# Optimization experiments

Hardware: AMD Instinct MI355X
Metric: run time of the kernel (lower is better)

Reference implementation:

```python
import jax, jax.numpy as jnp
import numpy as np
import math

B, S, D = 4, 2048, 1024
H, DK, DV = 16, 64, 64
EPS = 1e-5
SCALE = math.sqrt(1.0 / D)  # NOTE: original scales by 1/sqrt(d_model), not 1/sqrt(d_k)


def setup_inputs() -> dict:
    key = jax.random.key(0)
    ks = jax.random.split(key, 12)
    s = 0.02
    return {
        "Q": jax.random.normal(ks[0], (B, S, D), jnp.float32),
        "K": jax.random.normal(ks[1], (B, S, D), jnp.float32),
        "V": jax.random.normal(ks[2], (B, S, D), jnp.float32),
        # stacked per-head projection weights (torch Linear: y = x @ W.T + b)
        "Wq": jax.random.normal(ks[3], (H, D, DK), jnp.float32) * s,
        "bq": jnp.zeros((H, DK), jnp.float32),
        "Wk": jax.random.normal(ks[4], (H, D, DK), jnp.float32) * s,
        "bk": jnp.zeros((H, DK), jnp.float32),
        "Wv": jax.random.normal(ks[5], (H, D, DV), jnp.float32) * s,
        "bv": jnp.zeros((H, DV), jnp.float32),
        "Wo": jax.random.normal(ks[6], (H * DV, D), jnp.float32) * s,
        "bo": jnp.zeros((D,), jnp.float32),
        "gamma": jnp.ones((D,), jnp.float32),
        "beta": jnp.zeros((D,), jnp.float32),
    }


def reference(Q, K, V, Wq, bq, Wk, bk, Wv, bv, Wo, bo, gamma, beta):
    residual = Q
    # batched per-head projections: [B,S,D] x [H,D,dk] -> [B,H,S,dk]
    q = jnp.einsum("bsd,hdk->bhsk", Q, Wq) + bq[None, :, None, :]
    k = jnp.einsum("bsd,hdk->bhsk", K, Wk) + bk[None, :, None, :]
    v = jnp.einsum("bsd,hdv->bhsv", V, Wv) + bv[None, :, None, :]
    # scaled dot-product attention (scale uses d_model, per original code)
    attn = jax.nn.softmax(jnp.einsum("bhsk,bhtk->bhst", q, k) * SCALE, axis=-1)
    out = jnp.einsum("bhst,bhtv->bhsv", attn, v)  # [B,H,S,DV]
    # concat heads along feature dim: [B,S,H*DV]
    out = out.transpose(0, 2, 1, 3).reshape(B, S, H * DV)
    out = out @ Wo + bo  # output projection
    # dropout is identity in eval mode
    out = out + residual
    # BatchNorm1d over (B,S) per channel (training-mode batch stats)
    mean = jnp.mean(out, axis=(0, 1))
    var = jnp.mean(jnp.square(out - mean), axis=(0, 1))
    out = (out - mean) * jax.lax.rsqrt(var + EPS) * gamma + beta
    return out.transpose(0, 2, 1)  # (B, d_model, S)
```

## Files before the change

kernel.cpp:

```cpp
#include <hip/hip_runtime.h>

#define B_ 4
#define S_ 2048
#define D_ 1024
#define H_ 16
#define SCALE_ 0.03125f
#define EPS_ 1e-5f
#define NBS_ 8192

typedef unsigned short ushort_t;
typedef __attribute__((ext_vector_type(8))) short short8;
typedef __attribute__((ext_vector_type(4))) short short4v;
typedef __attribute__((ext_vector_type(4))) float floatx4;
typedef __attribute__((ext_vector_type(2))) unsigned int uint2v;

__device__ __forceinline__ ushort_t f2bf(float f) {
  union { float f; unsigned u; } v; v.f = f;
  unsigned r = v.u + 0x7fffu + ((v.u >> 16) & 1u);
  return (ushort_t)(r >> 16);
}

__device__ __forceinline__ float fast_exp2(float x) {
#if __has_builtin(__builtin_amdgcn_exp2f)
  return __builtin_amdgcn_exp2f(x);
#else
  return __expf(x * 0.6931471805599453f);
#endif
}

__device__ __forceinline__ unsigned cvt_pk_bf16(float a, float b) {
  unsigned r;
  asm("v_cvt_pk_bf16_f32 %0, %1, %2" : "=v"(r) : "v"(a), "v"(b));
  return r;
}

__device__ __forceinline__ short8 cvt8(float4 a, float4 b) {
  short8 r;
  r[0] = (short)f2bf(a.x); r[1] = (short)f2bf(a.y);
  r[2] = (short)f2bf(a.z); r[3] = (short)f2bf(a.w);
  r[4] = (short)f2bf(b.x); r[5] = (short)f2bf(b.y);
  r[6] = (short)f2bf(b.z); r[7] = (short)f2bf(b.w);
  return r;
}

__device__ __forceinline__ void gload16(const void* g, void* l) {
  __builtin_amdgcn_global_load_lds(
      (const __attribute__((address_space(1))) unsigned int*)g,
      (__attribute__((address_space(3))) unsigned int*)l, 16, 0, 0);
}

__global__ __launch_bounds__(256) void cvtx_k(const float* __restrict__ src,
                                              ushort_t* __restrict__ dst)
{
  size_t i = ((size_t)blockIdx.x * 256 + threadIdx.x) * 8;
  float4 a = *(const float4*)(src + i);
  float4 b = *(const float4*)(src + i + 4);
  *(short8*)(dst + i) = cvt8(a, b);
}

__global__ __launch_bounds__(256) void wtr_k(const float* __restrict__ src,
                                             ushort_t* __restrict__ dst, int mode)
{
  __shared__ float t[64][65];
  const int tr = blockIdx.x, tc = blockIdx.y;
  const float* sb; int sld;
  if (mode == 0) { sb = src + (size_t)tr * 65536 + (size_t)tc * 64 * 64; sld = 64; }
  else           { sb = src + (size_t)tc * 64 * 1024 + (size_t)tr * 64;  sld = 1024; }
  const int tid = threadIdx.x;
  const int rr = tid >> 2, cs = (tid & 3) * 16;
  const float* p = sb + (size_t)rr * sld + cs;
#pragma unroll
  for (int j = 0; j < 16; ++j) t[rr][cs + j] = p[j];
  __syncthreads();
  ushort_t* dp = dst + (size_t)(tr * 64 + rr) * 1024 + tc * 64 + cs;
#pragma unroll
  for (int j = 0; j < 16; ++j) dp[j] = f2bf(t[cs + j][rr]);
}

__global__ __launch_bounds__(256) void gemm_proj(
    const ushort_t* __restrict__ A, const ushort_t* __restrict__ Bw,
    const float* __restrict__ bias, ushort_t* __restrict__ outp, float scale)
{
  __shared__ ushort_t As[128 * 32];
  __shared__ ushort_t Bs[128 * 32];
  const int tid = threadIdx.x;
  const int wv = tid >> 6, lane = tid & 63, quad = lane >> 4, l16 = lane & 15;
  const int m0 = blockIdx.x * 128, n0 = blockIdx.y * 128;
  const int wm = wv & 1, wn = wv >> 1;
  const int lrow = lane >> 2, lkc = (lane & 3) * 8;

  floatx4 acc[4][4];
#pragma unroll
  for (int i = 0; i < 4; ++i)
#pragma unroll
    for (int j = 0; j < 4; ++j) acc[i][j] = (floatx4){0.f, 0.f, 0.f, 0.f};

  for (int k0 = 0; k0 < 1024; k0 += 32) {
    __syncthreads();
#pragma unroll
    for (int j = 0; j < 2; ++j) {
      const int rb = wv * 32 + j * 16;
      gload16(A + (size_t)(m0 + rb + lrow) * 1024 + k0 + lkc, (char*)As + rb * 64);
      gload16(Bw + (size_t)(n0 + rb + lrow) * 1024 + k0 + lkc, (char*)Bs + rb * 64);
    }
    __syncthreads();
    short8 af[4], bf[4];
#pragma unroll
    for (int i = 0; i < 4; ++i)
      af[i] = *(const short8*)&As[(wm * 64 + i * 16 + l16) * 32 + quad * 8];
#pragma unroll
    for (int i = 0; i < 4; ++i)
      bf[i] = *(const short8*)&Bs[(wn * 64 + i * 16 + l16) * 32 + quad * 8];
#pragma unroll
    for (int mi = 0; mi < 4; ++mi)
#pragma unroll
      for (int ni = 0; ni < 4; ++ni)
        acc[mi][ni] = __builtin_amdgcn_mfma_f32_16x16x32_bf16(
            af[mi], bf[ni], acc[mi][ni], 0, 0, 0);
  }

  const int b = m0 >> 11;
  const int sbase = (m0 & 2047) + wm * 64;
#pragma unroll
  for (int ni = 0; ni < 4; ++ni) {
    const int c = n0 + wn * 64 + ni * 16 + l16;
    const int h = c >> 6, nn = c & 63;
    const float bs = bias[c];
    ushort_t* op = outp + (size_t)(b * 16 + h) * 2048 * 64 + nn;
#pragma unroll
    for (int mi = 0; mi < 4; ++mi)
#pragma unroll
      for (int r = 0; r < 4; ++r) {
        int s = sbase + mi * 16 + quad * 4 + r;
        op[(size_t)s * 64] = f2bf((acc[mi][ni][r] + bs) * scale);
      }
  }
}

__global__ __launch_bounds__(256) void gemm_projT(
    const ushort_t* __restrict__ A, const ushort_t* __restrict__ Bw,
    const float* __restrict__ bias, ushort_t* __restrict__ outp)
{
  __shared__ ushort_t As[128 * 32];
  __shared__ ushort_t Bs[128 * 32];
  const int tid = threadIdx.x;
  const int wv = tid >> 6, lane = tid & 63, quad = lane >> 4, l16 = lane & 15;
  const int m0 = blockIdx.x * 128, n0 = blockIdx.y * 128;
  const int wm = wv & 1, wn = wv >> 1;
  const int lrow = lane >> 2, lkc = (lane & 3) * 8;

  floatx4 acc[4][4];
#pragma unroll
  for (int i = 0; i < 4; ++i)
#pragma unroll
    for (int j = 0; j < 4; ++j) acc[i][j] = (floatx4){0.f, 0.f, 0.f, 0.f};

  for (int k0 = 0; k0 < 1024; k0 += 32) {
    __syncthreads();
#pragma unroll
    for (int j = 0; j < 2; ++j) {
      const int rb = wv * 32 + j * 16;
      gload16(A + (size_t)(m0 + rb + lrow) * 1024 + k0 + lkc, (char*)As + rb * 64);
      gload16(Bw + (size_t)(n0 + rb + lrow) * 1024 + k0 + lkc, (char*)Bs + rb * 64);
    }
    __syncthreads();
    short8 af[4], bf[4];
#pragma unroll
    for (int i = 0; i < 4; ++i)
      af[i] = *(const short8*)&As[(wm * 64 + i * 16 + l16) * 32 + quad * 8];
#pragma unroll
    for (int i = 0; i < 4; ++i)
      bf[i] = *(const short8*)&Bs[(wn * 64 + i * 16 + l16) * 32 + quad * 8];
#pragma unroll
    for (int mi = 0; mi < 4; ++mi)
#pragma unroll
      for (int ni = 0; ni < 4; ++ni)
        acc[mi][ni] = __builtin_amdgcn_mfma_f32_16x16x32_bf16(
            af[mi], bf[ni], acc[mi][ni], 0, 0, 0);
  }

  const int b = m0 >> 11;
  const int sbase = (m0 & 2047) + wm * 64;
#pragma unroll
  for (int ni = 0; ni < 4; ++ni) {
    const int c = n0 + wn * 64 + ni * 16 + l16;
    const int h = c >> 6, nn = c & 63;
    const float bs = bias[c];
    ushort_t* op = outp + ((size_t)(b * 16 + h) * 64 + nn) * 2048;
#pragma unroll
    for (int mi = 0; mi < 4; ++mi) {
      int s0v = sbase + mi * 16 + quad * 4;
      short4v p;
#pragma unroll
      for (int r = 0; r < 4; ++r) p[r] = (short)f2bf(acc[mi][ni][r] + bs);
      *(short4v*)(op + s0v) = p;
    }
  }
}

__global__ __launch_bounds__(256) void gemm_oproj(
    const ushort_t* __restrict__ A, const ushort_t* __restrict__ Bw,
    const float* __restrict__ bo, const float* __restrict__ resid,
    float* __restrict__ y)
{
  __shared__ ushort_t As[128 * 32];
  __shared__ ushort_t Bs[128 * 32];
  const int tid = threadIdx.x;
  const int wv = tid >> 6, lane = tid & 63, quad = lane >> 4, l16 = lane & 15;
  const int m0 = blockIdx.x * 128, n0 = blockIdx.y * 128;
  const int wm = wv & 1, wn = wv >> 1;
  const int lrow = lane >> 2, lkc = (lane & 3) * 8;

  floatx4 acc[4][4];
#pragma unroll
  for (int i = 0; i < 4; ++i)
#pragma unroll
    for (int j = 0; j < 4; ++j) acc[i][j] = (floatx4){0.f, 0.f, 0.f, 0.f};

  for (int k0 = 0; k0 < 1024; k0 += 32) {
    __syncthreads();
#pragma unroll
    for (int j = 0; j < 2; ++j) {
      const int rb = wv * 32 + j * 16;
      gload16(A + (size_t)(m0 + rb + lrow) * 1024 + k0 + lkc, (char*)As + rb * 64);
      gload16(Bw + (size_t)(n0 + rb + lrow) * 1024 + k0 + lkc, (char*)Bs + rb * 64);
    }
    __syncthreads();
    short8 af[4], bf[4];
#pragma unroll
    for (int i = 0; i < 4; ++i)
      af[i] = *(const short8*)&As[(wm * 64 + i * 16 + l16) * 32 + quad * 8];
#pragma unroll
    for (int i = 0; i < 4; ++i)
      bf[i] = *(const short8*)&Bs[(wn * 64 + i * 16 + l16) * 32 + quad * 8];
#pragma unroll
    for (int mi = 0; mi < 4; ++mi)
#pragma unroll
      for (int ni = 0; ni < 4; ++ni)
        acc[mi][ni] = __builtin_amdgcn_mfma_f32_16x16x32_bf16(
            af[mi], bf[ni], acc[mi][ni], 0, 0, 0);
  }

  const int mb = m0 + wm * 64;
#pragma unroll
  for (int ni = 0; ni < 4; ++ni) {
    const int d = n0 + wn * 64 + ni * 16 + l16;
    const float bs = bo[d];
#pragma unroll
    for (int mi = 0; mi < 4; ++mi)
#pragma unroll
      for (int r = 0; r < 4; ++r) {
        int m = mb + mi * 16 + quad * 4 + r;
        y[(size_t)m * 1024 + d] = acc[mi][ni][r] + bs + resid[(size_t)m * 1024 + d];
      }
  }
}

__global__ __launch_bounds__(256, 3) void attn_k(
    const ushort_t* __restrict__ q, const ushort_t* __restrict__ k,
    const ushort_t* __restrict__ vt, ushort_t* __restrict__ ao)
{
  __shared__ ushort_t lds[24576];
  char* ldsb = (char*)lds;
  const int tid = threadIdx.x;
  const int wv = tid >> 6, lane = tid & 63, quad = lane >> 4, l16 = lane & 15;
  const int q0 = blockIdx.x * 128, h = blockIdx.y, b = blockIdx.z;
  const size_t bh = (size_t)(b * H_ + h) * S_;
  const ushort_t* vb = vt + (size_t)(b * H_ + h) * 64 * S_;

  short8 aq[2][2];
#pragma unroll
  for (int rb = 0; rb < 2; ++rb) {
    const ushort_t* qrow = q + (bh + q0 + wv * 32 + rb * 16 + l16) * 64;
    aq[rb][0] = *(const short8*)(qrow + quad * 8);
    aq[rb][1] = *(const short8*)(qrow + 32 + quad * 8);
  }

  short8 ones;
#pragma unroll
  for (int j = 0; j < 8; ++j) ones[j] = (short)0x3F80;

  floatx4 o[2][4];
  floatx4 accl[2];
#pragma unroll
  for (int rb = 0; rb < 2; ++rb) {
#pragma unroll
    for (int cb = 0; cb < 4; ++cb) o[rb][cb] = (floatx4){0.f, 0.f, 0.f, 0.f};
    accl[rb] = (floatx4){0.f, 0.f, 0.f, 0.f};
  }

  const int swz = ((l16 & 7) << 4) | (l16 & 8);
  const int q8 = quad * 8;
  const int pb = 32768 + wv * 4096 + l16 * 128;

  auto stage = [&](int nb, int t0) {
#pragma unroll
    for (int i = 0; i < 4; ++i) {
      const int idx = wv * 4 + i;
      const int cb = (idx >> 1) & 3, hf = idx & 1;
      if (idx < 8)
        gload16(k + (bh + t0 + cb * 16 + l16) * 64 + hf * 32 + quad * 8,
                (char*)lds + nb * 8192 + idx * 1024);
      else
        gload16(vb + (size_t)(cb * 16 + l16) * S_ + t0 + hf * 32 + quad * 8,
                (char*)lds + 16384 + nb * 8192 + (idx - 8) * 1024);
    }
  };

  stage(0, 0);
  asm volatile("s_waitcnt vmcnt(0)" ::: "memory");
  __syncthreads();

  for (int t0 = 0; t0 < S_; t0 += 64) {
    const int nb = (t0 >> 6) & 1;
    const ushort_t* KsC = lds + nb * 4096;
    const ushort_t* VsC = lds + 8192 + nb * 4096;
    if (t0 + 64 < S_) stage(nb ^ 1, t0 + 64);

    floatx4 sc[2][4];
#pragma unroll
    for (int rb = 0; rb < 2; ++rb)
#pragma unroll
      for (int cb = 0; cb < 4; ++cb) sc[rb][cb] = (floatx4){0.f, 0.f, 0.f, 0.f};
    __builtin_amdgcn_s_setprio(1);
#pragma unroll
    for (int hf = 0; hf < 2; ++hf) {
      short8 bk[4];
#pragma unroll
      for (int cb = 0; cb < 4; ++cb)
        bk[cb] = *(const short8*)&KsC[(cb * 2 + hf) * 512 + lane * 8];
#pragma unroll
      for (int rb = 0; rb < 2; ++rb)
#pragma unroll
        for (int cb = 0; cb < 4; ++cb)
          sc[rb][cb] = __builtin_amdgcn_mfma_f32_16x16x32_bf16(
              bk[cb], aq[rb][hf], sc[rb][cb], 0, 0, 0);
    }
    __builtin_amdgcn_s_setprio(0);

    short8 bvf[2][4];
#pragma unroll
    for (int hf = 0; hf < 2; ++hf)
#pragma unroll
      for (int cb = 0; cb < 4; ++cb)
        bvf[hf][cb] = *(const short8*)&VsC[(cb * 2 + hf) * 512 + lane * 8];

#pragma unroll
    for (int rb = 0; rb < 2; ++rb)
#pragma unroll
      for (int cb = 0; cb < 4; ++cb) {
        float p0 = fast_exp2(sc[rb][cb][0]);
        float p1 = fast_exp2(sc[rb][cb][1]);
        float p2 = fast_exp2(sc[rb][cb][2]);
        float p3 = fast_exp2(sc[rb][cb][3]);
        uint2v w;
        w[0] = cvt_pk_bf16(p0, p1);
        w[1] = cvt_pk_bf16(p2, p3);
        *(uint2v*)(ldsb + pb + rb * 2048 + ((cb * 32 + q8) ^ swz)) = w;
      }
    asm volatile("s_waitcnt lgkmcnt(0)" ::: "memory");
    __builtin_amdgcn_sched_barrier(0);

    __builtin_amdgcn_s_setprio(1);
#pragma unroll
    for (int rb = 0; rb < 2; ++rb)
#pragma unroll
      for (int hf = 0; hf < 2; ++hf) {
        const char* pr = ldsb + pb + rb * 2048;
        const int lo = (hf * 64 + quad * 16) ^ swz;
        short4v a0 = *(const short4v*)(pr + lo);
        short4v a1 = *(const short4v*)(pr + (lo ^ 8));
        short8 ap;
        ap[0] = a0[0]; ap[1] = a0[1]; ap[2] = a0[2]; ap[3] = a0[3];
        ap[4] = a1[0]; ap[5] = a1[1]; ap[6] = a1[2]; ap[7] = a1[3];
#pragma unroll
        for (int cb = 0; cb < 4; ++cb)
          o[rb][cb] = __builtin_amdgcn_mfma_f32_16x16x32_bf16(
              ap, bvf[hf][cb], o[rb][cb], 0, 0, 0);
        accl[rb] = __builtin_amdgcn_mfma_f32_16x16x32_bf16(
            ap, ones, accl[rb], 0, 0, 0);
      }
    __builtin_amdgcn_s_setprio(0);

    asm volatile("s_waitcnt vmcnt(0)" ::: "memory");
    __syncthreads();
  }

  float linv[2][4];
#pragma unroll
  for (int rb = 0; rb < 2; ++rb)
#pragma unroll
    for (int r = 0; r < 4; ++r)
      linv[rb][r] = 1.f / accl[rb][r];
#pragma unroll
  for (int rb = 0; rb < 2; ++rb)
#pragma unroll
    for (int cb = 0; cb < 4; ++cb)
#pragma unroll
      for (int r = 0; r < 4; ++r) {
        float val = o[rb][cb][r] * linv[rb][r];
        size_t idx = (size_t)(b * S_ + q0 + wv * 32 + rb * 16 + quad * 4 + r) * 1024
                     + h * 64 + cb * 16 + l16;
        ao[idx] = f2bf(val);
      }
}

__global__ __launch_bounds__(256) void stats_k(
    const float* __restrict__ y, float* __restrict__ s1, float* __restrict__ s2)
{
  const int tid = threadIdx.x;
  const int r0 = blockIdx.x * 32;
  float a[4] = {0.f, 0.f, 0.f, 0.f}, bb[4] = {0.f, 0.f, 0.f, 0.f};
  for (int r = 0; r < 32; ++r) {
    const float* row = y + (size_t)(r0 + r) * D_;
#pragma unroll
    for (int j = 0; j < 4; ++j) {
      float vv = row[tid + j * 256];
      a[j] += vv;
      bb[j] += vv * vv;
    }
  }
#pragma unroll
  for (int j = 0; j < 4; ++j) {
    atomicAdd(&s1[tid + j * 256], a[j]);
    atomicAdd(&s2[tid + j * 256], bb[j]);
  }
}

__global__ __launch_bounds__(256) void norm_k(
    const float* __restrict__ y, const float* __restrict__ s1,
    const float* __restrict__ s2, const float* __restrict__ gamma,
    const float* __restrict__ beta, float* __restrict__ out)
{
  __shared__ float tile[64][65];
  __shared__ float scl[64], sft[64];
  const int tid = threadIdx.x;
  const int s0 = blockIdx.x * 64, d0 = blockIdx.y * 64, b = blockIdx.z;

  if (tid < 64) {
    int d = d0 + tid;
    float mean = s1[d] * (1.f / (float)NBS_);
    float var = s2[d] * (1.f / (float)NBS_) - mean * mean;
    float rstd = rsqrtf(var + EPS_);
    float g = gamma[d];
    scl[tid] = rstd * g;
    sft[tid] = beta[d] - mean * rstd * g;
  }
  __syncthreads();

  const int si = tid >> 2, dc = (tid & 3) * 16;
  const float* row = y + (size_t)(b * S_ + s0 + si) * D_ + d0 + dc;
#pragma unroll
  for (int j = 0; j < 16; ++j)
    tile[si][dc + j] = row[j] * scl[dc + j] + sft[dc + j];
  __syncthreads();

  const int di = tid >> 2, sg = (tid & 3) * 16;
  float* dst = out + (size_t)(b * D_ + d0 + di) * S_ + s0 + sg;
#pragma unroll
  for (int jj = 0; jj < 4; ++jj) {
    float4 p;
    p.x = tile[sg + jj * 4 + 0][di];
    p.y = tile[sg + jj * 4 + 1][di];
    p.z = tile[sg + jj * 4 + 2][di];
    p.w = tile[sg + jj * 4 + 3][di];
    *(float4*)(dst + jj * 4) = p;
  }
}

extern "C" void kernel_launch(void* const* d_in, const int* in_sizes, int n_in,
                              void* d_out, int out_size, void* d_ws, size_t ws_size,
                              hipStream_t stream)
{
  (void)in_sizes; (void)n_in; (void)out_size; (void)ws_size;
  const float* Q     = (const float*)d_in[0];
  const float* Kin   = (const float*)d_in[1];
  const float* Vin   = (const float*)d_in[2];
  const float* Wq    = (const float*)d_in[3];
  const float* bq    = (const float*)d_in[4];
  const float* Wk    = (const float*)d_in[5];
  const float* bk    = (const float*)d_in[6];
  const float* Wv    = (const float*)d_in[7];
  const float* bv    = (const float*)d_in[8];
  const float* Wo    = (const float*)d_in[9];
  const float* bo    = (const float*)d_in[10];
  const float* gamma = (const float*)d_in[11];
  const float* beta  = (const float*)d_in[12];
  float* out = (float*)d_out;

  char* ws = (char*)d_ws;
  const size_t MB = 1u << 20;
  ushort_t* xb  = (ushort_t*)(ws);
  ushort_t* wtq = (ushort_t*)(ws + 16 * MB);
  ushort_t* wtk = (ushort_t*)(ws + 18 * MB);
  ushort_t* wtv = (ushort_t*)(ws + 20 * MB);
  ushort_t* wto = (ushort_t*)(ws + 22 * MB);
  ushort_t* qb  = (ushort_t*)(ws + 24 * MB);
  ushort_t* kb  = (ushort_t*)(ws + 40 * MB);
  ushort_t* vtb = (ushort_t*)(ws + 56 * MB);
  ushort_t* ao  = (ushort_t*)(ws);
  float*    y   = (float*)(ws + 24 * MB);
  float*    s1  = (float*)(ws + 56 * MB);
  float*    s2  = (float*)(ws + 56 * MB + 4096);

  wtr_k<<<dim3(16, 16), 256, 0, stream>>>(Wq, wtq, 0);
  wtr_k<<<dim3(16, 16), 256, 0, stream>>>(Wk, wtk, 0);
  wtr_k<<<dim3(16, 16), 256, 0, stream>>>(Wv, wtv, 0);
  wtr_k<<<dim3(16, 16), 256, 0, stream>>>(Wo, wto, 1);

  const float QSC = SCALE_ * 1.44269504088896f;
  cvtx_k<<<4096, 256, 0, stream>>>(Q, xb);
  gemm_proj<<<dim3(64, 8), 256, 0, stream>>>(xb, wtq, bq, qb, QSC);
  cvtx_k<<<4096, 256, 0, stream>>>(Kin, xb);
  gemm_proj<<<dim3(64, 8), 256, 0, stream>>>(xb, wtk, bk, kb, 1.0f);
  cvtx_k<<<4096, 256, 0, stream>>>(Vin, xb);
  gemm_projT<<<dim3(64, 8), 256, 0, stream>>>(xb, wtv, bv, vtb);

  attn_k<<<dim3(16, 16, 4), 256, 0, stream>>>(qb, kb, vtb, ao);
  gemm_oproj<<<dim3(64, 8), 256, 0, stream>>>(ao, wto, bo, Q, y);

  hipMemsetAsync(ws + 56 * MB, 0, 8192, stream);
  stats_k<<<256, 256, 0, stream>>>(y, s1, s2);
  norm_k<<<dim3(32, 16, 4), 256, 0, stream>>>(y, s1, s2, gamma, beta, out);
}
```

Before: 400.6 us.

## Double-buffer GEMM mainloop with swizzled LDS and fuse batchnorm stats into output projection

Replaces the three GEMM mainloops with a shared double-buffered loop using a K-tile of 64 and an XOR-swizzled LDS layout, so the next tile's global loads overlap the current tile's MFMAs and LDS bank conflicts drop. It also folds the per-channel sum and sum-of-squares into the output-projection epilogue via shuffles and atomics, which removes the separate stats kernel and its re-read of y. The cost is 64KB of LDS per GEMM block, which may reduce occupancy, and more atomic traffic from the epilogue.

```diff
diff --git a/kernel.cpp b/kernel.cpp
--- a/kernel.cpp
+++ b/kernel.cpp
@@ -77,17 +77,67 @@
   for (int j = 0; j < 16; ++j) dp[j] = f2bf(t[cs + j][rr]);
 }
 
+__device__ __forceinline__ void gemm_mainloop(
+    const ushort_t* __restrict__ A, const ushort_t* __restrict__ Bw,
+    ushort_t* As, ushort_t* Bs,
+    int m0, int n0, int wv, int lane, floatx4 acc[4][4])
+{
+  const int quad = lane >> 4, l16 = lane & 15;
+  const int wm = wv & 1, wn = wv >> 1;
+  const int r8 = lane >> 3;
+  const int kx = ((lane & 7) ^ r8) * 8;
+
+  auto stage = [&](int buf, int k0) {
+#pragma unroll
+    for (int j = 0; j < 4; ++j) {
+      const int rb = (wv * 4 + j) * 8;
+      gload16(A + (size_t)(m0 + rb + r8) * 1024 + k0 + kx,
+              (char*)As + buf * 16384 + rb * 128);
+      gload16(Bw + (size_t)(n0 + rb + r8) * 1024 + k0 + kx,
+              (char*)Bs + buf * 16384 + rb * 128);
+    }
+  };
+
+  stage(0, 0);
+  __syncthreads();
+
+  const int swz = (l16 & 7) << 4;
+  for (int it = 0; it < 16; ++it) {
+    const int cur = it & 1;
+    if (it < 15) stage(cur ^ 1, (it + 1) * 64);
+    const char* Ab = (const char*)As + cur * 16384;
+    const char* Bb = (const char*)Bs + cur * 16384;
+#pragma unroll
+    for (int hf = 0; hf < 2; ++hf) {
+      short8 af[4], bf[4];
+      const int C = (hf * 64 + quad * 16) ^ swz;
+#pragma unroll
+      for (int i = 0; i < 4; ++i)
+        af[i] = *(const short8*)(Ab + (wm * 64 + i * 16 + l16) * 128 + C);
+#pragma unroll
+      for (int i = 0; i < 4; ++i)
+        bf[i] = *(const short8*)(Bb + (wn * 64 + i * 16 + l16) * 128 + C);
+#pragma unroll
+      for (int mi = 0; mi < 4; ++mi)
+#pragma unroll
+        for (int ni = 0; ni < 4; ++ni)
+          acc[mi][ni] = __builtin_amdgcn_mfma_f32_16x16x32_bf16(
+              af[mi], bf[ni], acc[mi][ni], 0, 0, 0);
+    }
+    __syncthreads();
+  }
+}
+
 __global__ __launch_bounds__(256) void gemm_proj(
     const ushort_t* __restrict__ A, const ushort_t* __restrict__ Bw,
     const float* __restrict__ bias, ushort_t* __restrict__ outp, float scale)
 {
-  __shared__ ushort_t As[128 * 32];
-  __shared__ ushort_t Bs[128 * 32];
+  __shared__ ushort_t As[2 * 128 * 64];
+  __shared__ ushort_t Bs[2 * 128 * 64];
   const int tid = threadIdx.x;
   const int wv = tid >> 6, lane = tid & 63, quad = lane >> 4, l16 = lane & 15;
   const int m0 = blockIdx.x * 128, n0 = blockIdx.y * 128;
   const int wm = wv & 1, wn = wv >> 1;
-  const int lrow = lane >> 2, lkc = (lane & 3) * 8;
 
   floatx4 acc[4][4];
 #pragma unroll
@@ -95,29 +145,7 @@
 #pragma unroll
     for (int j = 0; j < 4; ++j) acc[i][j] = (floatx4){0.f, 0.f, 0.f, 0.f};
 
-  for (int k0 = 0; k0 < 1024; k0 += 32) {
-    __syncthreads();
-#pragma unroll
-    for (int j = 0; j < 2; ++j) {
-      const int rb = wv * 32 + j * 16;
-      gload16(A + (size_t)(m0 + rb + lrow) * 1024 + k0 + lkc, (char*)As + rb * 64);
-      gload16(Bw + (size_t)(n0 + rb + lrow) * 1024 + k0 + lkc, (char*)Bs + rb * 64);
-    }
-    __syncthreads();
-    short8 af[4], bf[4];
-#pragma unroll
-    for (int i = 0; i < 4; ++i)
-      af[i] = *(const short8*)&As[(wm * 64 + i * 16 + l16) * 32 + quad * 8];
-#pragma unroll
-    for (int i = 0; i < 4; ++i)
-      bf[i] = *(const short8*)&Bs[(wn * 64 + i * 16 + l16) * 32 + quad * 8];
-#pragma unroll
-    for (int mi = 0; mi < 4; ++mi)
-#pragma unroll
-      for (int ni = 0; ni < 4; ++ni)
-        acc[mi][ni] = __builtin_amdgcn_mfma_f32_16x16x32_bf16(
-            af[mi], bf[ni], acc[mi][ni], 0, 0, 0);
-  }
+  gemm_mainloop(A, Bw, As, Bs, m0, n0, wv, lane, acc);
 
   const int b = m0 >> 11;
   const int sbase = (m0 & 2047) + wm * 64;
@@ -141,13 +169,12 @@
     const ushort_t* __restrict__ A, const ushort_t* __restrict__ Bw,
     const float* __restrict__ bias, ushort_t* __restrict__ outp)
 {
-  __shared__ ushort_t As[128 * 32];
-  __shared__ ushort_t Bs[128 * 32];
+  __shared__ ushort_t As[2 * 128 * 64];
+  __shared__ ushort_t Bs[2 * 128 * 64];
   const int tid = threadIdx.x;
   const int wv = tid >> 6, lane = tid & 63, quad = lane >> 4, l16 = lane & 15;
   const int m0 = blockIdx.x * 128, n0 = blockIdx.y * 128;
   const int wm = wv & 1, wn = wv >> 1;
-  const int lrow = lane >> 2, lkc = (lane & 3) * 8;
 
   floatx4 acc[4][4];
 #pragma unroll
@@ -155,29 +182,7 @@
 #pragma unroll
     for (int j = 0; j < 4; ++j) acc[i][j] = (floatx4){0.f, 0.f, 0.f, 0.f};
 
-  for (int k0 = 0; k0 < 1024; k0 += 32) {
-    __syncthreads();
-#pragma unroll
-    for (int j = 0; j < 2; ++j) {
-      const int rb = wv * 32 + j * 16;
-      gload16(A + (size_t)(m0 + rb + lrow) * 1024 + k0 + lkc, (char*)As + rb * 64);
-      gload16(Bw + (size_t)(n0 + rb + lrow) * 1024 + k0 + lkc, (char*)Bs + rb * 64);
-    }
-    __syncthreads();
-    short8 af[4], bf[4];
-#pragma unroll
-    for (int i = 0; i < 4; ++i)
-      af[i] = *(const short8*)&As[(wm * 64 + i * 16 + l16) * 32 + quad * 8];
-#pragma unroll
-    for (int i = 0; i < 4; ++i)
-      bf[i] = *(const short8*)&Bs[(wn * 64 + i * 16 + l16) * 32 + quad * 8];
-#pragma unroll
-    for (int mi = 0; mi < 4; ++mi)
-#pragma unroll
-      for (int ni = 0; ni < 4; ++ni)
-        acc[mi][ni] = __builtin_amdgcn_mfma_f32_16x16x32_bf16(
-            af[mi], bf[ni], acc[mi][ni], 0, 0, 0);
-  }
+  gemm_mainloop(A, Bw, As, Bs, m0, n0, wv, lane, acc);
 
   const int b = m0 >> 11;
   const int sbase = (m0 & 2047) + wm * 64;
@@ -201,15 +206,14 @@
 __global__ __launch_bounds__(256) void gemm_oproj(
     const ushort_t* __restrict__ A, const ushort_t* __restrict__ Bw,
     const float* __restrict__ bo, const float* __restrict__ resid,
-    float* __restrict__ y)
-{
-  __shared__ ushort_t As[128 * 32];
-  __shared__ ushort_t Bs[128 * 32];
+    float* __restrict__ y, float* __restrict__ s1, float* __restrict__ s2)
+{
+  __shared__ ushort_t As[2 * 128 * 64];
+  __shared__ ushort_t Bs[2 * 128 * 64];
   const int tid = threadIdx.x;
   const int wv = tid >> 6, lane = tid & 63, quad = lane >> 4, l16 = lane & 15;
   const int m0 = blockIdx.x * 128, n0 = blockIdx.y * 128;
   const int wm = wv & 1, wn = wv >> 1;
-  const int lrow = lane >> 2, lkc = (lane & 3) * 8;
 
   floatx4 acc[4][4];
 #pragma unroll
@@ -217,42 +221,30 @@
 #pragma unroll
     for (int j = 0; j < 4; ++j) acc[i][j] = (floatx4){0.f, 0.f, 0.f, 0.f};
 
-  for (int k0 = 0; k0 < 1024; k0 += 32) {
-    __syncthreads();
-#pragma unroll
-    for (int j = 0; j < 2; ++j) {
-      const int rb = wv * 32 + j * 16;
-      gload16(A + (size_t)(m0 + rb + lrow) * 1024 + k0 + lkc, (char*)As + rb * 64);
-      gload16(Bw + (size_t)(n0 + rb + lrow) * 1024 + k0 + lkc, (char*)Bs + rb * 64);
-    }
-    __syncthreads();
-    short8 af[4], bf[4];
-#pragma unroll
-    for (int i = 0; i < 4; ++i)
-      af[i] = *(const short8*)&As[(wm * 64 + i * 16 + l16) * 32 + quad * 8];
-#pragma unroll
-    for (int i = 0; i < 4; ++i)
-      bf[i] = *(const short8*)&Bs[(wn * 64 + i * 16 + l16) * 32 + quad * 8];
-#pragma unroll
-    for (int mi = 0; mi < 4; ++mi)
-#pragma unroll
-      for (int ni = 0; ni < 4; ++ni)
-        acc[mi][ni] = __builtin_amdgcn_mfma_f32_16x16x32_bf16(
-            af[mi], bf[ni], acc[mi][ni], 0, 0, 0);
-  }
+  gemm_mainloop(A, Bw, As, Bs, m0, n0, wv, lane, acc);
 
   const int mb = m0 + wm * 64;
 #pragma unroll
   for (int ni = 0; ni < 4; ++ni) {
     const int d = n0 + wn * 64 + ni * 16 + l16;
     const float bs = bo[d];
+    float ps1 = 0.f, ps2 = 0.f;
 #pragma unroll
     for (int mi = 0; mi < 4; ++mi)
 #pragma unroll
       for (int r = 0; r < 4; ++r) {
         int m = mb + mi * 16 + quad * 4 + r;
-        y[(size_t)m * 1024 + d] = acc[mi][ni][r] + bs + resid[(size_t)m * 1024 + d];
+        float val = acc[mi][ni][r] + bs + resid[(size_t)m * 1024 + d];
+        y[(size_t)m * 1024 + d] = val;
+        ps1 += val;
+        ps2 += val * val;
       }
+    ps1 += __shfl_xor(ps1, 16); ps1 += __shfl_xor(ps1, 32);
+    ps2 += __shfl_xor(ps2, 16); ps2 += __shfl_xor(ps2, 32);
+    if (quad == 0) {
+      atomicAdd(&s1[d], ps1);
+      atomicAdd(&s2[d], ps2);
+    }
   }
 }
 
@@ -403,28 +395,6 @@
                      + h * 64 + cb * 16 + l16;
         ao[idx] = f2bf(val);
       }
-}
-
-__global__ __launch_bounds__(256) void stats_k(
-    const float* __restrict__ y, float* __restrict__ s1, float* __restrict__ s2)
-{
-  const int tid = threadIdx.x;
-  const int r0 = blockIdx.x * 32;
-  float a[4] = {0.f, 0.f, 0.f, 0.f}, bb[4] = {0.f, 0.f, 0.f, 0.f};
-  for (int r = 0; r < 32; ++r) {
-    const float* row = y + (size_t)(r0 + r) * D_;
-#pragma unroll
-    for (int j = 0; j < 4; ++j) {
-      float vv = row[tid + j * 256];
-      a[j] += vv;
-      bb[j] += vv * vv;
-    }
-  }
-#pragma unroll
-  for (int j = 0; j < 4; ++j) {
-    atomicAdd(&s1[tid + j * 256], a[j]);
-    atomicAdd(&s2[tid + j * 256], bb[j]);
-  }
 }
 
 __global__ __launch_bounds__(256) void norm_k(
@@ -517,9 +487,9 @@
   gemm_projT<<<dim3(64, 8), 256, 0, stream>>>(xb, wtv, bv, vtb);
 
   attn_k<<<dim3(16, 16, 4), 256, 0, stream>>>(qb, kb, vtb, ao);
-  gemm_oproj<<<dim3(64, 8), 256, 0, stream>>>(ao, wto, bo, Q, y);
 
   hipMemsetAsync(ws + 56 * MB, 0, 8192, stream);
-  stats_k<<<256, 256, 0, stream>>>(y, s1, s2);
+  gemm_oproj<<<dim3(64, 8), 256, 0, stream>>>(ao, wto, bo, Q, y, s1, s2);
+
   norm_k<<<dim3(32, 16, 4), 256, 0, stream>>>(y, s1, s2, gamma, beta, out);
 }
```

Measured after the change: 389.9 us. 2.7% less time.
